# Kernel optimization log

Measured on AMD Instinct MI355X. Metric: run time of the kernel, lower is better.

## Reference

```python
import jax, jax.numpy as jnp
import numpy as np

# DeepSeek-style MLA sparse decode: absorbed W_UK/W_UV matmuls in latent space,
# top-k sparse gather from the (kv_lora_rank + rope) latent KV cache.

B, H, S, K = 32, 16, 8192, 2048
L, DN, DR, DV, DM = 512, 128, 64, 128, 2048
SCALE = 1.0 / np.sqrt(DN + DR)  # softmax scale over full qk_head_dim = 192


def setup_inputs() -> dict:
    key = jax.random.key(0)
    ks = jax.random.split(key, 8)
    return {
        "q_nope": jax.random.normal(ks[0], (B, H, DN), dtype=jnp.float32),
        "q_pe": jax.random.normal(ks[1], (B, H, DR), dtype=jnp.float32),  # post-RoPE
        "kv_c": jax.random.normal(ks[2], (B, S, L), dtype=jnp.float32),   # latent cache
        "k_pe": jax.random.normal(ks[3], (B, S, DR), dtype=jnp.float32),  # post-RoPE cache
        "W_UK": jax.random.normal(ks[4], (L, H, DN), dtype=jnp.float32) * 0.02,
        "W_UV": jax.random.normal(ks[5], (L, H, DV), dtype=jnp.float32) * 0.02,
        "W_O": jax.random.normal(ks[6], (H * DV, DM), dtype=jnp.float32) * 0.02,
        "topk_indices": jax.random.randint(ks[7], (B, K), 0, S, dtype=jnp.int32),
    }


def reference(q_nope, q_pe, kv_c, k_pe, W_UK, W_UV, W_O, topk_indices):
    b, h, _ = q_nope.shape
    seq = kv_c.shape[1]
    # absorb q_nope into latent space: [B,H,L]
    q_latent = jnp.einsum('bhd,lhd->bhl', q_nope, W_UK)
    # top-k sparse gather from paged latent cache (-1 == invalid slot)
    valid = topk_indices >= 0                         # [B,K]
    idx = jnp.clip(topk_indices, 0, seq - 1)
    kv_sel = jnp.take_along_axis(kv_c, idx[:, :, None], axis=1)   # [B,K,L]
    kpe_sel = jnp.take_along_axis(k_pe, idx[:, :, None], axis=1)  # [B,K,DR]
    # attention scores: latent part + rope part, fused scale
    scores = (jnp.einsum('bhl,bkl->bhk', q_latent, kv_sel)
              + jnp.einsum('bhr,bkr->bhk', q_pe, kpe_sel)) * SCALE
    scores = jnp.where(valid[:, None, :], scores, -jnp.inf)
    attn = jax.nn.softmax(scores, axis=-1)            # [B,H,K]
    # weighted sum in latent space, then up-project with W_UV
    o_latent = jnp.einsum('bhk,bkl->bhl', attn, kv_sel)
    o = jnp.einsum('bhl,lhv->bhv', o_latent, W_UV)    # [B,H,DV]
    return o.reshape(b, h * o.shape[-1]) @ W_O        # [B,DM]
```

## Files before the change

### kernel.cpp

```cpp
#include <hip/hip_runtime.h>
#include <hip/hip_bf16.h>
#include <cstdint>
#include <cstddef>

constexpr int NB = 32;
constexpr int NH = 16;
constexpr int NS = 8192;
constexpr int NK = 2048;
constexpr int NL = 512;
constexpr int NDR = 64;
constexpr int NDV = 128;
constexpr int NDM = 2048;
constexpr int NDN = 128;
constexpr float SCALE = 0.07216878364870322f;

constexpr int NSPLIT = 32;
constexpr int KC = NK / NSPLIT;
constexpr int ND = NL + NDR;
constexpr int NSUB_D = ND / 16;
constexpr int NS2 = 64;

typedef __attribute__((ext_vector_type(8))) short sh8;
typedef __attribute__((ext_vector_type(4))) float f32x4;

__device__ __forceinline__ short bf16c(float f) {
  union { float f; uint32_t u; } v; v.f = f;
  uint32_t r = v.u + 0x7fffu + ((v.u >> 16) & 1u);
  return (short)(r >> 16);
}

__device__ __forceinline__ float bf2f(short s) {
  union { uint32_t u; float f; } v; v.u = ((uint32_t)(uint16_t)s) << 16;
  return v.f;
}

__device__ __forceinline__ sh8 pack_bf8(float4 a, float4 b) {
  sh8 f;
  f[0] = bf16c(a.x); f[1] = bf16c(a.y); f[2] = bf16c(a.z); f[3] = bf16c(a.w);
  f[4] = bf16c(b.x); f[5] = bf16c(b.y); f[6] = bf16c(b.z); f[7] = bf16c(b.w);
  return f;
}

__global__ __launch_bounds__(256)
void k_qprep(const float* __restrict__ qn,
             const float* __restrict__ qpe,
             const float* __restrict__ wuk,
             short* __restrict__ qle) {
  const int h  = blockIdx.x & 15;
  const int lc = blockIdx.x >> 4;
  const int l0 = lc * 32;
  const int t  = threadIdx.x;
  __shared__ float wlds[32 * 136];
  __shared__ float qlds[32 * 136];

  #pragma unroll
  for (int j = 0; j < 4; ++j) {
    int idx = t + j * 256;
    int li  = idx >> 5;
    int d4  = (idx & 31) * 4;
    *(float4*)&wlds[li * 136 + d4] =
        *(const float4*)&wuk[((size_t)(l0 + li) * NH + h) * NDN + d4];
    *(float4*)&qlds[li * 136 + d4] =
        *(const float4*)&qn[((size_t)li * NH + h) * NDN + d4];
  }
  __syncthreads();

  const int b = t >> 3;
  #pragma unroll
  for (int j = 0; j < 4; ++j) {
    int li = (t & 7) + j * 8;
    float acc = 0.f;
    #pragma unroll
    for (int d4 = 0; d4 < NDN; d4 += 4) {
      float4 wv = *(float4*)&wlds[li * 136 + d4];
      float4 qv = *(float4*)&qlds[b * 136 + d4];
      acc += wv.x * qv.x + wv.y * qv.y + wv.z * qv.z + wv.w * qv.w;
    }
    qle[((size_t)b * NH + h) * ND + l0 + li] = bf16c(acc);
  }
  if (lc == 0) {
    #pragma unroll
    for (int j = 0; j < 8; ++j) {
      int i = t + j * 256;
      int bb = i >> 6, dr = i & 63;
      qle[((size_t)bb * NH + h) * ND + NL + dr] =
          bf16c(qpe[((size_t)bb * NH + h) * NDR + dr]);
    }
  }
}

__global__ __launch_bounds__(256, 2)
void k_attn(const float* __restrict__ kvc,
            const float* __restrict__ kpe,
            const int*   __restrict__ topk,
            const short* __restrict__ qle,
            float* __restrict__ pm,
            float* __restrict__ psum,
            unsigned short* __restrict__ po) {
  const int sp = blockIdx.x;
  const int b  = blockIdx.y;
  const int t  = threadIdx.x;
  const int w  = t >> 6;
  const int lane = t & 63;
  const int lg = lane >> 4;
  const int ln = lane & 15;

  __shared__ __align__(16) short kvs[(KC / 4) * NSUB_D * 64];
  __shared__ __align__(16) short plds[NH * 72];
  __shared__ float mlds[4 * NH];
  __shared__ float slds[4 * NH];

  {
    const int r = t >> 2, c8 = t & 3;
    int idx = topk[(size_t)b * NK + sp * KC + r];
    int id = idx < 0 ? 0 : (idx >= NS ? NS - 1 : idx);
    const float* rowc = kvc + ((size_t)b * NS + id) * NL;
    const float* rowp = kpe + ((size_t)b * NS + id) * NDR;
    #pragma unroll
    for (int g = 0; g < 3; ++g) {
      float4 va[6], vb[6];
      #pragma unroll
      for (int i = 0; i < 6; ++i) {
        int d0 = c8 * 8 + (g * 6 + i) * 32;
        const float* src = (d0 < NL) ? (rowc + d0) : (rowp + (d0 - NL));
        va[i] = *(const float4*)src;
        vb[i] = *(const float4*)(src + 4);
      }
      #pragma unroll
      for (int i = 0; i < 6; ++i) {
        int d0 = c8 * 8 + (g * 6 + i) * 32;
        int s = (r >> 2) * NSUB_D + (d0 >> 4);
        *(sh8*)&kvs[s * 64 + (r & 3) * 16 + (d0 & 15)] = pack_bf8(va[i], vb[i]);
      }
    }
  }
  __syncthreads();

  f32x4 accs = {0.f, 0.f, 0.f, 0.f};
  {
    const short* qrow = qle + ((size_t)b * NH + ln) * ND;
    int k = w * 16 + ln;
    int kbase = (k >> 2) * NSUB_D * 64 + (k & 3) * 16;
    #pragma unroll
    for (int kk = 0; kk < 18; ++kk) {
      int d0 = kk * 32 + lg * 8;
      sh8 qv = *(const sh8*)&qrow[d0];
      sh8 bfr = *(const sh8*)&kvs[kbase + (d0 >> 4) * 64 + (d0 & 15)];
      accs = __builtin_amdgcn_mfma_f32_16x16x32_bf16(qv, bfr, accs, 0, 0, 0);
    }
  }

  const int kq = w * 16 + ln;
  bool valid = topk[(size_t)b * NK + sp * KC + kq] >= 0;
  float sv[4], mx[4];
  #pragma unroll
  for (int q = 0; q < 4; ++q) {
    sv[q] = valid ? accs[q] * SCALE : -INFINITY;
    mx[q] = sv[q];
  }
  #pragma unroll
  for (int off = 1; off < 16; off <<= 1)
    #pragma unroll
    for (int q = 0; q < 4; ++q) mx[q] = fmaxf(mx[q], __shfl_xor(mx[q], off));
  if (ln == 0) {
    #pragma unroll
    for (int q = 0; q < 4; ++q) mlds[w * NH + lg * 4 + q] = mx[q];
  }
  __syncthreads();

  float pr[4], sm[4];
  #pragma unroll
  for (int q = 0; q < 4; ++q) {
    int h = lg * 4 + q;
    float m = fmaxf(fmaxf(mlds[h], mlds[NH + h]),
                    fmaxf(mlds[2 * NH + h], mlds[3 * NH + h]));
    m = fmaxf(m, -1e30f);
    pr[q] = __expf(sv[q] - m);
    sm[q] = pr[q];
  }
  #pragma unroll
  for (int off = 1; off < 16; off <<= 1)
    #pragma unroll
    for (int q = 0; q < 4; ++q) sm[q] += __shfl_xor(sm[q], off);
  if (ln == 0) {
    #pragma unroll
    for (int q = 0; q < 4; ++q) slds[w * NH + lg * 4 + q] = sm[q];
  }
  #pragma unroll
  for (int q = 0; q < 4; ++q)
    plds[(lg * 4 + q) * 72 + kq] = bf16c(pr[q]);
  __syncthreads();

  if (t < NH) {
    float m = fmaxf(fmaxf(mlds[t], mlds[NH + t]),
                    fmaxf(mlds[2 * NH + t], mlds[3 * NH + t]));
    m = fmaxf(m, -1e30f);
    float s = slds[t] + slds[NH + t] + slds[2 * NH + t] + slds[3 * NH + t];
    pm[((size_t)b * NSPLIT + sp) * NH + t] = m;
    psum[((size_t)b * NSPLIT + sp) * NH + t] = s;
  }

  f32x4 acco[8];
  #pragma unroll
  for (int nt = 0; nt < 8; ++nt) acco[nt] = {0.f, 0.f, 0.f, 0.f};

  #pragma unroll
  for (int ks = 0; ks < 2; ++ks) {
    sh8 pa = *(const sh8*)&plds[ln * 72 + ks * 32 + lg * 8];
    int kb = ks * 32 + lg * 8;
    #pragma unroll
    for (int nt = 0; nt < 8; ++nt) {
      int l0 = w * 128 + nt * 16;
      int s = (kb >> 2) * NSUB_D + (l0 >> 4);
      const short* base = &kvs[s * 64 + ln];
      sh8 bv;
      #pragma unroll
      for (int j = 0; j < 4; ++j) bv[j] = base[j * 16];
      #pragma unroll
      for (int j = 0; j < 4; ++j) bv[4 + j] = base[NSUB_D * 64 + j * 16];
      acco[nt] = __builtin_amdgcn_mfma_f32_16x16x32_bf16(pa, bv, acco[nt], 0, 0, 0);
    }
  }

  unsigned short* dst = po + (((size_t)b * NSPLIT + sp) * NH) * NL;
  #pragma unroll
  for (int nt = 0; nt < 8; ++nt) {
    int l = w * 128 + nt * 16 + ln;
    #pragma unroll
    for (int q = 0; q < 4; ++q)
      dst[(size_t)(lg * 4 + q) * NL + l] = (unsigned short)bf16c(acco[nt][q]);
  }
}

__global__ __launch_bounds__(256)
void k_combine(const float* __restrict__ pm,
               const float* __restrict__ psum,
               const unsigned short* __restrict__ po,
               const float* __restrict__ wuv,
               float* __restrict__ ov) {
  int bh = blockIdx.x;
  int b = bh >> 4, h = bh & 15;
  __shared__ float clds[NSPLIT];
  __shared__ float ol[NL];
  __shared__ float red[2][NDV];
  int t = threadIdx.x;
  if (t < NSPLIT) {
    float m = pm[((size_t)b * NSPLIT + t) * NH + h];
    float M = m;
    #pragma unroll
    for (int off = 16; off; off >>= 1) M = fmaxf(M, __shfl_xor(M, off, 32));
    float term = psum[((size_t)b * NSPLIT + t) * NH + h] * __expf(m - M);
    float S = term;
    #pragma unroll
    for (int off = 16; off; off >>= 1) S += __shfl_xor(S, off, 32);
    clds[t] = __expf(m - M) / fmaxf(S, 1e-30f);
  }
  __syncthreads();
  {
    float a0 = 0.f, a1 = 0.f;
    #pragma unroll
    for (int i = 0; i < NSPLIT; ++i) {
      uint32_t pv = *(const uint32_t*)&po[(((size_t)b * NSPLIT + i) * NH + h) * NL + 2 * t];
      a0 += clds[i] * bf2f((short)(pv & 0xffff));
      a1 += clds[i] * bf2f((short)(pv >> 16));
    }
    ol[2 * t] = a0;
    ol[2 * t + 1] = a1;
  }
  __syncthreads();
  {
    int v = t & (NDV - 1);
    int half = t >> 7;
    float a = 0.f;
    #pragma unroll 16
    for (int l = half * 256; l < half * 256 + 256; ++l)
      a += ol[l] * wuv[((size_t)l * NH + h) * NDV + v];
    red[half][v] = a;
  }
  __syncthreads();
  if (t < NDV) ov[(size_t)bh * NDV + t] = red[0][t] + red[1][t];
}

__global__ __launch_bounds__(256)
void k_gemm_atomic(const float* __restrict__ ov,
                   const float* __restrict__ wo,
                   float* __restrict__ out) {
  int mc = blockIdx.x;
  int ns = blockIdx.y;
  __shared__ float oc[NB * 32];
  int t = threadIdx.x;
  for (int i = t; i < NB * 32; i += 256) {
    int b = i >> 5, n = i & 31;
    oc[i] = ov[(size_t)b * NDM + ns * 32 + n];
  }
  __syncthreads();
  float acc[NB];
  #pragma unroll
  for (int b = 0; b < NB; ++b) acc[b] = 0.f;
  int m = mc * 256 + t;
  #pragma unroll 8
  for (int n = 0; n < 32; ++n) {
    float wv = wo[(size_t)(ns * 32 + n) * NDM + m];
    #pragma unroll
    for (int b = 0; b < NB; ++b) acc[b] += oc[b * 32 + n] * wv;
  }
  #pragma unroll
  for (int b = 0; b < NB; ++b)
    atomicAdd(&out[(size_t)b * NDM + m], acc[b]);
}

extern "C" void kernel_launch(void* const* d_in, const int* in_sizes, int n_in,
                              void* d_out, int out_size, void* d_ws, size_t ws_size,
                              hipStream_t stream) {
  const float* q_nope = (const float*)d_in[0];
  const float* q_pe   = (const float*)d_in[1];
  const float* kv_c   = (const float*)d_in[2];
  const float* k_pe   = (const float*)d_in[3];
  const float* W_UK   = (const float*)d_in[4];
  const float* W_UV   = (const float*)d_in[5];
  const float* W_O    = (const float*)d_in[6];
  const int*   topk   = (const int*)d_in[7];
  float* out = (float*)d_out;

  float* ws = (float*)d_ws;
  short* qle = (short*)ws;
  float* pm   = ws + 147456;
  float* psum = pm + 16384;
  unsigned short* po = (unsigned short*)(psum + 16384);
  float* ov   = psum + 16384 + 4194304;

  hipMemsetAsync(d_out, 0, (size_t)out_size * sizeof(float), stream);
  k_qprep<<<256, 256, 0, stream>>>(q_nope, q_pe, W_UK, qle);
  k_attn<<<dim3(NSPLIT, NB), 256, 0, stream>>>(kv_c, k_pe, topk, qle,
                                               pm, psum, po);
  k_combine<<<NB * NH, 256, 0, stream>>>(pm, psum, po, W_UV, ov);
  k_gemm_atomic<<<dim3(8, NS2), 256, 0, stream>>>(ov, W_O, out);
}
```

Before: 94.08 us.

## Double attention split count, raise occupancy, fold output zeroing into qprep

Doubles the number of key splits per batch so each attention block handles 32 keys instead of 64. This gives more blocks and a smaller LDS footprint, and launch bounds now allow four blocks per CU. The score phase now uses only two waves, and the combine kernel reduces over 64 partials with full-wave shuffles. The output memset is folded into the qprep kernel, removing one launch. The trade-off is twice as much partial-output traffic and a larger workspace, with half the waves idle during the score computation.

```diff
diff --git a/kernel.cpp b/kernel.cpp
--- a/kernel.cpp
+++ b/kernel.cpp
@@ -14,7 +14,7 @@
 constexpr int NDN = 128;
 constexpr float SCALE = 0.07216878364870322f;
 
-constexpr int NSPLIT = 32;
+constexpr int NSPLIT = 64;
 constexpr int KC = NK / NSPLIT;
 constexpr int ND = NL + NDR;
 constexpr int NSUB_D = ND / 16;
@@ -45,13 +45,16 @@
 void k_qprep(const float* __restrict__ qn,
              const float* __restrict__ qpe,
              const float* __restrict__ wuk,
-             short* __restrict__ qle) {
+             short* __restrict__ qle,
+             float* __restrict__ out) {
   const int h  = blockIdx.x & 15;
   const int lc = blockIdx.x >> 4;
   const int l0 = lc * 32;
   const int t  = threadIdx.x;
   __shared__ float wlds[32 * 136];
   __shared__ float qlds[32 * 136];
+
+  out[(size_t)blockIdx.x * 256 + t] = 0.f;
 
   #pragma unroll
   for (int j = 0; j < 4; ++j) {
@@ -89,7 +92,7 @@
   }
 }
 
-__global__ __launch_bounds__(256, 2)
+__global__ __launch_bounds__(256, 4)
 void k_attn(const float* __restrict__ kvc,
             const float* __restrict__ kpe,
             const int*   __restrict__ topk,
@@ -106,38 +109,36 @@
   const int ln = lane & 15;
 
   __shared__ __align__(16) short kvs[(KC / 4) * NSUB_D * 64];
-  __shared__ __align__(16) short plds[NH * 72];
-  __shared__ float mlds[4 * NH];
-  __shared__ float slds[4 * NH];
+  __shared__ __align__(16) short plds[NH * 40];
+  __shared__ float mlds[2 * NH];
+  __shared__ float slds[2 * NH];
 
   {
-    const int r = t >> 2, c8 = t & 3;
+    const int r = t >> 3, c8 = t & 7;
     int idx = topk[(size_t)b * NK + sp * KC + r];
     int id = idx < 0 ? 0 : (idx >= NS ? NS - 1 : idx);
     const float* rowc = kvc + ((size_t)b * NS + id) * NL;
     const float* rowp = kpe + ((size_t)b * NS + id) * NDR;
-    #pragma unroll
-    for (int g = 0; g < 3; ++g) {
-      float4 va[6], vb[6];
-      #pragma unroll
-      for (int i = 0; i < 6; ++i) {
-        int d0 = c8 * 8 + (g * 6 + i) * 32;
-        const float* src = (d0 < NL) ? (rowc + d0) : (rowp + (d0 - NL));
-        va[i] = *(const float4*)src;
-        vb[i] = *(const float4*)(src + 4);
-      }
-      #pragma unroll
-      for (int i = 0; i < 6; ++i) {
-        int d0 = c8 * 8 + (g * 6 + i) * 32;
-        int s = (r >> 2) * NSUB_D + (d0 >> 4);
-        *(sh8*)&kvs[s * 64 + (r & 3) * 16 + (d0 & 15)] = pack_bf8(va[i], vb[i]);
-      }
-    }
-  }
-  __syncthreads();
-
-  f32x4 accs = {0.f, 0.f, 0.f, 0.f};
-  {
+    float4 va[9], vb[9];
+    #pragma unroll
+    for (int i = 0; i < 9; ++i) {
+      int d0 = c8 * 8 + i * 64;
+      const float* src = (d0 < NL) ? (rowc + d0) : (rowp + (d0 - NL));
+      va[i] = *(const float4*)src;
+      vb[i] = *(const float4*)(src + 4);
+    }
+    #pragma unroll
+    for (int i = 0; i < 9; ++i) {
+      int d0 = c8 * 8 + i * 64;
+      int s = (r >> 2) * NSUB_D + (d0 >> 4);
+      *(sh8*)&kvs[s * 64 + (r & 3) * 16 + (d0 & 15)] = pack_bf8(va[i], vb[i]);
+    }
+  }
+  __syncthreads();
+
+  float sv[4];
+  if (w < 2) {
+    f32x4 accs = {0.f, 0.f, 0.f, 0.f};
     const short* qrow = qle + ((size_t)b * NH + ln) * ND;
     int k = w * 16 + ln;
     int kbase = (k >> 2) * NSUB_D * 64 + (k & 3) * 16;
@@ -148,54 +149,52 @@
       sh8 bfr = *(const sh8*)&kvs[kbase + (d0 >> 4) * 64 + (d0 & 15)];
       accs = __builtin_amdgcn_mfma_f32_16x16x32_bf16(qv, bfr, accs, 0, 0, 0);
     }
-  }
-
-  const int kq = w * 16 + ln;
-  bool valid = topk[(size_t)b * NK + sp * KC + kq] >= 0;
-  float sv[4], mx[4];
-  #pragma unroll
-  for (int q = 0; q < 4; ++q) {
-    sv[q] = valid ? accs[q] * SCALE : -INFINITY;
-    mx[q] = sv[q];
-  }
-  #pragma unroll
-  for (int off = 1; off < 16; off <<= 1)
-    #pragma unroll
-    for (int q = 0; q < 4; ++q) mx[q] = fmaxf(mx[q], __shfl_xor(mx[q], off));
-  if (ln == 0) {
-    #pragma unroll
-    for (int q = 0; q < 4; ++q) mlds[w * NH + lg * 4 + q] = mx[q];
-  }
-  __syncthreads();
-
-  float pr[4], sm[4];
-  #pragma unroll
-  for (int q = 0; q < 4; ++q) {
-    int h = lg * 4 + q;
-    float m = fmaxf(fmaxf(mlds[h], mlds[NH + h]),
-                    fmaxf(mlds[2 * NH + h], mlds[3 * NH + h]));
-    m = fmaxf(m, -1e30f);
-    pr[q] = __expf(sv[q] - m);
-    sm[q] = pr[q];
-  }
-  #pragma unroll
-  for (int off = 1; off < 16; off <<= 1)
-    #pragma unroll
-    for (int q = 0; q < 4; ++q) sm[q] += __shfl_xor(sm[q], off);
-  if (ln == 0) {
-    #pragma unroll
-    for (int q = 0; q < 4; ++q) slds[w * NH + lg * 4 + q] = sm[q];
-  }
-  #pragma unroll
-  for (int q = 0; q < 4; ++q)
-    plds[(lg * 4 + q) * 72 + kq] = bf16c(pr[q]);
+    const int kq = w * 16 + ln;
+    bool valid = topk[(size_t)b * NK + sp * KC + kq] >= 0;
+    float mx[4];
+    #pragma unroll
+    for (int q = 0; q < 4; ++q) {
+      sv[q] = valid ? accs[q] * SCALE : -INFINITY;
+      mx[q] = sv[q];
+    }
+    #pragma unroll
+    for (int off = 1; off < 16; off <<= 1)
+      #pragma unroll
+      for (int q = 0; q < 4; ++q) mx[q] = fmaxf(mx[q], __shfl_xor(mx[q], off));
+    if (ln == 0) {
+      #pragma unroll
+      for (int q = 0; q < 4; ++q) mlds[w * NH + lg * 4 + q] = mx[q];
+    }
+  }
+  __syncthreads();
+
+  if (w < 2) {
+    const int kq = w * 16 + ln;
+    float pr[4], sm[4];
+    #pragma unroll
+    for (int q = 0; q < 4; ++q) {
+      int h = lg * 4 + q;
+      float m = fmaxf(fmaxf(mlds[h], mlds[NH + h]), -1e30f);
+      pr[q] = __expf(sv[q] - m);
+      sm[q] = pr[q];
+    }
+    #pragma unroll
+    for (int off = 1; off < 16; off <<= 1)
+      #pragma unroll
+      for (int q = 0; q < 4; ++q) sm[q] += __shfl_xor(sm[q], off);
+    if (ln == 0) {
+      #pragma unroll
+      for (int q = 0; q < 4; ++q) slds[w * NH + lg * 4 + q] = sm[q];
+    }
+    #pragma unroll
+    for (int q = 0; q < 4; ++q)
+      plds[(lg * 4 + q) * 40 + kq] = bf16c(pr[q]);
+  }
   __syncthreads();
 
   if (t < NH) {
-    float m = fmaxf(fmaxf(mlds[t], mlds[NH + t]),
-                    fmaxf(mlds[2 * NH + t], mlds[3 * NH + t]));
-    m = fmaxf(m, -1e30f);
-    float s = slds[t] + slds[NH + t] + slds[2 * NH + t] + slds[3 * NH + t];
+    float m = fmaxf(fmaxf(mlds[t], mlds[NH + t]), -1e30f);
+    float s = slds[t] + slds[NH + t];
     pm[((size_t)b * NSPLIT + sp) * NH + t] = m;
     psum[((size_t)b * NSPLIT + sp) * NH + t] = s;
   }
@@ -203,16 +202,12 @@
   f32x4 acco[8];
   #pragma unroll
   for (int nt = 0; nt < 8; ++nt) acco[nt] = {0.f, 0.f, 0.f, 0.f};
-
-  #pragma unroll
-  for (int ks = 0; ks < 2; ++ks) {
-    sh8 pa = *(const sh8*)&plds[ln * 72 + ks * 32 + lg * 8];
-    int kb = ks * 32 + lg * 8;
+  {
+    sh8 pa = *(const sh8*)&plds[ln * 40 + lg * 8];
     #pragma unroll
     for (int nt = 0; nt < 8; ++nt) {
       int l0 = w * 128 + nt * 16;
-      int s = (kb >> 2) * NSUB_D + (l0 >> 4);
-      const short* base = &kvs[s * 64 + ln];
+      const short* base = &kvs[(lg * 2) * NSUB_D * 64 + (l0 >> 4) * 64 + ln];
       sh8 bv;
       #pragma unroll
       for (int j = 0; j < 4; ++j) bv[j] = base[j * 16];
@@ -248,11 +243,11 @@
     float m = pm[((size_t)b * NSPLIT + t) * NH + h];
     float M = m;
     #pragma unroll
-    for (int off = 16; off; off >>= 1) M = fmaxf(M, __shfl_xor(M, off, 32));
+    for (int off = 32; off; off >>= 1) M = fmaxf(M, __shfl_xor(M, off));
     float term = psum[((size_t)b * NSPLIT + t) * NH + h] * __expf(m - M);
     float S = term;
     #pragma unroll
-    for (int off = 16; off; off >>= 1) S += __shfl_xor(S, off, 32);
+    for (int off = 32; off; off >>= 1) S += __shfl_xor(S, off);
     clds[t] = __expf(m - M) / fmaxf(S, 1e-30f);
   }
   __syncthreads();
@@ -325,12 +320,11 @@
   float* ws = (float*)d_ws;
   short* qle = (short*)ws;
   float* pm   = ws + 147456;
-  float* psum = pm + 16384;
-  unsigned short* po = (unsigned short*)(psum + 16384);
-  float* ov   = psum + 16384 + 4194304;
-
-  hipMemsetAsync(d_out, 0, (size_t)out_size * sizeof(float), stream);
-  k_qprep<<<256, 256, 0, stream>>>(q_nope, q_pe, W_UK, qle);
+  float* psum = pm + 32768;
+  unsigned short* po = (unsigned short*)(psum + 32768);
+  float* ov   = psum + 32768 + 8388608;
+
+  k_qprep<<<256, 256, 0, stream>>>(q_nope, q_pe, W_UK, qle, out);
   k_attn<<<dim3(NSPLIT, NB), 256, 0, stream>>>(kv_c, k_pe, topk, qle,
                                                pm, psum, po);
   k_combine<<<NB * NH, 256, 0, stream>>>(pm, psum, po, W_UV, ov);
```

Result: faster. 87.18 us (-7.3%).
